# Optimization experiments

Measured on AMD Instinct MI355X. Metric: run time of the kernel, lower is better.

Reference implementation:

```python
import jax, jax.numpy as jnp
import numpy as np

N_NODES = 100000
N_EDGES = 1600000
D = 128


def setup_inputs() -> dict:
    key = jax.random.key(0)
    k1, k2, k3, k4, k5 = jax.random.split(key, 5)
    x = jax.random.normal(k1, (N_NODES, D), dtype=jnp.float32)
    edge_index = jax.random.randint(k2, (2, N_EDGES), 0, N_NODES, dtype=jnp.int32)
    edge_weight = jax.random.uniform(k3, (N_EDGES,), dtype=jnp.float32)
    W_lin = jax.random.normal(k4, (D, D), dtype=jnp.float32) / np.sqrt(D)
    W_gcn = jax.random.normal(k5, (D, D), dtype=jnp.float32) / np.sqrt(D)
    return {"x": x, "edge_index": edge_index, "edge_weight": edge_weight,
            "W_lin": W_lin, "W_gcn": W_gcn}


def reference(x, edge_index, edge_weight, W_lin, W_gcn):
    # hl = Linear(x) (no bias)
    hl = x @ W_lin  # [N, D]

    # GCNConv with add_self_loops=False, normalize=True, no bias:
    row = edge_index[0]  # src
    col = edge_index[1]  # dst
    # symmetric gcn_norm from edge weights (degree scattered onto dst)
    deg = jax.ops.segment_sum(edge_weight, col, num_segments=x.shape[0])  # [N]
    deg_inv_sqrt = jnp.where(deg > 0, jax.lax.rsqrt(deg), 0.0)
    norm = deg_inv_sqrt[row] * edge_weight * deg_inv_sqrt[col]  # [E]

    h = x @ W_gcn  # [N, D] transform before propagate
    msg = h[row] * norm[:, None]  # [E, D] gather + scale
    hr = jax.ops.segment_sum(msg, col, num_segments=x.shape[0])  # scatter-add [N, D]

    return hl + hr
```

## Files before the change

kernel.cpp:

```cpp
#include <hip/hip_runtime.h>

#define NN 100000
#define NE 1600000
#define DD 128
#define NB 1563
#define HIST_BLKS 128
#define PB (HIST_BLKS / 64)
#define CAST_BLKS 752
#define WT2_BLKS  16
#define K1_BLKS (HIST_BLKS + CAST_BLKS + WT2_BLKS)
#define BINCAP 1536

typedef __attribute__((ext_vector_type(8))) short bf16x8;
typedef __attribute__((ext_vector_type(4))) float f32x4;

__device__ inline unsigned short f2bf(float f) {
  union { float f; unsigned u; } v; v.f = f;
  unsigned r = (v.u + 0x7FFF + ((v.u >> 16) & 1)) >> 16;
  return (unsigned short)r;
}

__global__ __launch_bounds__(512) void kb1(const int* __restrict__ col,
    const float* __restrict__ x, const float* __restrict__ Wl, const float* __restrict__ Wg,
    unsigned* __restrict__ hist, unsigned short* __restrict__ xb, unsigned short* __restrict__ WT2) {
  __shared__ unsigned h1[NB];
  int b = blockIdx.x, tid = threadIdx.x;
  if (b < HIST_BLKS) {
    for (int i = tid; i < NB; i += 512) h1[i] = 0;
    __syncthreads();
    for (int e = b * 512 + tid; e < NE; e += HIST_BLKS * 512)
      atomicAdd(&h1[((unsigned)col[e]) >> 6], 1u);
    __syncthreads();
    for (int i = tid; i < NB; i += 512) hist[(size_t)i * HIST_BLKS + b] = h1[i];
  } else if (b < HIST_BLKS + CAST_BLKS) {
    int bb = b - HIST_BLKS;
    const int total8 = NN * DD / 8;
    for (int i = bb * 512 + tid; i < total8; i += CAST_BLKS * 512) {
      float4 a = *(const float4*)&x[i * 8];
      float4 q = *(const float4*)&x[i * 8 + 4];
      unsigned short o[8] = {f2bf(a.x), f2bf(a.y), f2bf(a.z), f2bf(a.w),
                             f2bf(q.x), f2bf(q.y), f2bf(q.z), f2bf(q.w)};
      *(uint4*)&xb[i * 8] = *(uint4*)o;
    }
  } else {
    int bb = b - HIST_BLKS - CAST_BLKS;
    int j = bb * 8 + (tid >> 6);
    int l = tid & 63;
    for (int k = l; k < 256; k += 64) {
      const float* W = (k < DD) ? Wl : Wg;
      WT2[j * 256 + k] = f2bf(W[(k & (DD - 1)) * DD + j]);
    }
  }
}

__global__ __launch_bounds__(256) void kb2a(const unsigned* __restrict__ hist,
    unsigned* __restrict__ binTotal) {
  int w = (blockIdx.x * 256 + threadIdx.x) >> 6, l = threadIdx.x & 63;
  if (w >= NB) return;
  unsigned s = 0;
  for (int k = l; k < HIST_BLKS; k += 64) s += hist[(size_t)w * HIST_BLKS + k];
  #pragma unroll
  for (int off = 32; off >= 1; off >>= 1) s += __shfl_down(s, off, 64);
  if (l == 0) binTotal[w] = s;
}

__global__ __launch_bounds__(512) void kb2b(const unsigned* __restrict__ binTotal,
    unsigned* __restrict__ binBase) {
  __shared__ unsigned ps[512];
  int t = threadIdx.x;
  unsigned v[4], s = 0;
  #pragma unroll
  for (int k = 0; k < 4; k++) { int i = t * 4 + k; v[k] = (i < NB) ? binTotal[i] : 0; s += v[k]; }
  ps[t] = s;
  __syncthreads();
  for (int off = 1; off < 512; off <<= 1) {
    unsigned u = (t >= off) ? ps[t - off] : 0;
    __syncthreads();
    ps[t] += u;
    __syncthreads();
  }
  unsigned run = ps[t] - s;
  #pragma unroll
  for (int k = 0; k < 4; k++) { int i = t * 4 + k; if (i < NB + 1) binBase[i] = run; run += v[k]; }
}

__global__ __launch_bounds__(256) void kb2c(const unsigned* __restrict__ hist,
    const unsigned* __restrict__ binBase, unsigned* __restrict__ off) {
  int w = (blockIdx.x * 256 + threadIdx.x) >> 6, l = threadIdx.x & 63;
  if (w >= NB) return;
  unsigned v[PB], s = 0;
  #pragma unroll
  for (int k = 0; k < PB; k++) { v[k] = hist[(size_t)w * HIST_BLKS + l * PB + k]; s += v[k]; }
  unsigned incl = s;
  #pragma unroll
  for (int o = 1; o < 64; o <<= 1) { unsigned tt = __shfl_up(incl, o, 64); if (l >= o) incl += tt; }
  unsigned run = binBase[w] + incl - s;
  #pragma unroll
  for (int k = 0; k < PB; k++) { off[(size_t)(l * PB + k) * NB + w] = run; run += v[k]; }
}

__global__ __launch_bounds__(512) void kb3(const int* __restrict__ row, const int* __restrict__ col,
    const float* __restrict__ ew, const unsigned* __restrict__ off,
    unsigned long long* __restrict__ entries) {
  __shared__ unsigned cnt[NB];
  int b = blockIdx.x, tid = threadIdx.x;
  for (int i = tid; i < NB; i += 512) cnt[i] = off[(size_t)b * NB + i];
  __syncthreads();
  for (int e = b * 512 + tid; e < NE; e += HIST_BLKS * 512) {
    int c = col[e];
    unsigned pos = atomicAdd(&cnt[((unsigned)c) >> 6], 1u);
    entries[pos] = ((unsigned long long)__float_as_uint(ew[e]) << 32)
                 | ((unsigned)row[e] << 6) | (unsigned)(c & 63);
  }
}

__global__ __launch_bounds__(256) void kb4(const unsigned long long* __restrict__ entries,
    const unsigned* __restrict__ binBase, float* __restrict__ dis) {
  __shared__ unsigned degFx[64];
  int bin = blockIdx.x, tid = threadIdx.x;
  if (tid < 64) degFx[tid] = 0;
  __syncthreads();
  unsigned s0 = binBase[bin], n = binBase[bin + 1] - s0;
  for (unsigned i = tid; i < n; i += 256) {
    unsigned long long e = entries[s0 + i];
    float w = __uint_as_float((unsigned)(e >> 32));
    atomicAdd(&degFx[(unsigned)e & 63], (unsigned)(w * 67108864.0f + 0.5f));
  }
  __syncthreads();
  if (tid < 64) {
    int node = bin * 64 + tid;
    if (node < NN) {
      float d = (float)degFx[tid] * (1.0f / 67108864.0f);
      dis[node] = (d > 0.0f) ? rsqrtf(d) : 0.0f;
    }
  }
}

__global__ __launch_bounds__(512) void kb5(const unsigned long long* __restrict__ entries,
    const unsigned* __restrict__ binBase, const float* __restrict__ dis,
    const unsigned short* __restrict__ xb, unsigned short* __restrict__ yb) {
  __shared__ unsigned long long raw[BINCAP], srt[BINCAP];
  __shared__ unsigned short rnk[BINCAP];
  __shared__ unsigned cnt64[64];
  __shared__ unsigned base64[64];
  int bin = blockIdx.x, tid = threadIdx.x;
  unsigned s0 = binBase[bin];
  int n = (int)(binBase[bin + 1] - s0);
  if (n > BINCAP) n = BINCAP;
  if (tid < 64) cnt64[tid] = 0;
  for (int i = tid; i < n; i += 512) raw[i] = entries[s0 + i];
  __syncthreads();
  for (int i = tid; i < n; i += 512)
    rnk[i] = (unsigned short)atomicAdd(&cnt64[(unsigned)raw[i] & 63], 1u);
  __syncthreads();
  if (tid < 64) {
    unsigned v = cnt64[tid], incl = v;
    #pragma unroll
    for (int o = 1; o < 64; o <<= 1) { unsigned t2 = __shfl_up(incl, o, 64); if (tid >= o) incl += t2; }
    base64[tid] = incl - v;
  }
  __syncthreads();
  for (int i = tid; i < n; i += 512) {
    unsigned long long e = raw[i];
    srt[base64[(unsigned)e & 63] + rnk[i]] = e;
  }
  __syncthreads();
  for (int i = tid; i < n; i += 512) {
    unsigned long long e = srt[i];
    unsigned src = ((unsigned)e) >> 6;
    float wn = __uint_as_float((unsigned)(e >> 32)) * dis[src];
    srt[i] = ((unsigned long long)__float_as_uint(wn) << 32) | (unsigned)(e & 0xFFFFFFFFu);
  }
  __syncthreads();
  int wv = tid >> 6, lane = tid & 63, grp = lane >> 4, l16 = lane & 15;
  for (int dd = 0; dd < 8; ++dd) {
    int d = wv * 8 + dd;
    int c = bin * 64 + d;
    if (c >= NN) break;
    int e0 = base64[d], m = cnt64[d];
    float acc[8] = {};
    for (int i = 0; i < m; i += 16) {
      int j0 = i + grp, j1 = i + 4 + grp, j2 = i + 8 + grp, j3 = i + 12 + grp;
      unsigned sA = 0, sB = 0, sC = 0, sD = 0;
      float wA = 0.f, wB = 0.f, wC = 0.f, wD = 0.f;
      if (j0 < m) { unsigned long long e = srt[e0 + j0]; sA = ((unsigned)e) >> 6; wA = __uint_as_float((unsigned)(e >> 32)); }
      if (j1 < m) { unsigned long long e = srt[e0 + j1]; sB = ((unsigned)e) >> 6; wB = __uint_as_float((unsigned)(e >> 32)); }
      if (j2 < m) { unsigned long long e = srt[e0 + j2]; sC = ((unsigned)e) >> 6; wC = __uint_as_float((unsigned)(e >> 32)); }
      if (j3 < m) { unsigned long long e = srt[e0 + j3]; sD = ((unsigned)e) >> 6; wD = __uint_as_float((unsigned)(e >> 32)); }
      uint4 qA = *(const uint4*)&xb[(size_t)sA * DD + l16 * 8];
      uint4 qB = *(const uint4*)&xb[(size_t)sB * DD + l16 * 8];
      uint4 qC = *(const uint4*)&xb[(size_t)sC * DD + l16 * 8];
      uint4 qD = *(const uint4*)&xb[(size_t)sD * DD + l16 * 8];
      union { uint4 v; unsigned u[4]; } ua, ub, uc, ud;
      ua.v = qA; ub.v = qB; uc.v = qC; ud.v = qD;
      #pragma unroll
      for (int k = 0; k < 4; k++) {
        union { unsigned u; float f; } lo, hi;
        lo.u = ua.u[k] << 16;          hi.u = ua.u[k] & 0xFFFF0000u;
        acc[2 * k] += wA * lo.f;       acc[2 * k + 1] += wA * hi.f;
        lo.u = ub.u[k] << 16;          hi.u = ub.u[k] & 0xFFFF0000u;
        acc[2 * k] += wB * lo.f;       acc[2 * k + 1] += wB * hi.f;
        lo.u = uc.u[k] << 16;          hi.u = uc.u[k] & 0xFFFF0000u;
        acc[2 * k] += wC * lo.f;       acc[2 * k + 1] += wC * hi.f;
        lo.u = ud.u[k] << 16;          hi.u = ud.u[k] & 0xFFFF0000u;
        acc[2 * k] += wD * lo.f;       acc[2 * k + 1] += wD * hi.f;
      }
    }
    #pragma unroll
    for (int k = 0; k < 8; k++) {
      acc[k] += __shfl_xor(acc[k], 16, 64);
      acc[k] += __shfl_xor(acc[k], 32, 64);
    }
    if (grp == 0) {
      float dc = dis[c];
      unsigned short o[8] = {f2bf(acc[0] * dc), f2bf(acc[1] * dc), f2bf(acc[2] * dc),
                             f2bf(acc[3] * dc), f2bf(acc[4] * dc), f2bf(acc[5] * dc),
                             f2bf(acc[6] * dc), f2bf(acc[7] * dc)};
      *(uint4*)&yb[(size_t)c * DD + l16 * 8] = *(uint4*)o;
    }
  }
}

__global__ __launch_bounds__(256) void k_gemm(const unsigned short* __restrict__ xb,
    const unsigned short* __restrict__ yb, const unsigned short* __restrict__ WT2,
    float* __restrict__ out, int N) {
  __shared__ __align__(16) unsigned short Bl[128 * 256];
  __shared__ __align__(16) unsigned short Al[64 * 256];
  int t = threadIdx.x;
  int rowbase = blockIdx.x * 64;

  const uint4* WTv = (const uint4*)WT2;
  #pragma unroll
  for (int i = 0; i < 16; i++) {
    int ci = t + i * 256;
    int j = ci >> 5, c16 = ci & 31;
    uint4 v = WTv[ci];
    int byte = j * 512 + c16 * 16;
    byte ^= (j & 7) << 4;
    *(uint4*)((char*)Bl + byte) = v;
  }
  #pragma unroll
  for (int i = 0; i < 8; i++) {
    int ci = t + i * 256;
    int r = ci >> 5, c16 = ci & 31;
    int gr = rowbase + r;
    uint4 v = make_uint4(0, 0, 0, 0);
    if (gr < N) {
      if (c16 < 16) v = *(const uint4*)&xb[(size_t)gr * DD + c16 * 8];
      else          v = *(const uint4*)&yb[(size_t)gr * DD + (c16 - 16) * 8];
    }
    int byte = r * 512 + c16 * 16;
    byte ^= (r & 7) << 4;
    *(uint4*)((char*)Al + byte) = v;
  }
  __syncthreads();

  int wid = t >> 6, lane = t & 63;
  int wn = wid * 32;
  int l15 = lane & 15, l4 = lane >> 4;
  f32x4 acc[4][2] = {};
  #pragma unroll
  for (int kk = 0; kk < 8; kk++) {
    bf16x8 af[4], bfr[2];
    #pragma unroll
    for (int m = 0; m < 4; m++) {
      int r = m * 16 + l15;
      int byte = r * 512 + kk * 64 + l4 * 16;
      byte ^= (r & 7) << 4;
      af[m] = *(const bf16x8*)((const char*)Al + byte);
    }
    #pragma unroll
    for (int n = 0; n < 2; n++) {
      int r = wn + n * 16 + l15;
      int byte = r * 512 + kk * 64 + l4 * 16;
      byte ^= (r & 7) << 4;
      bfr[n] = *(const bf16x8*)((const char*)Bl + byte);
    }
    #pragma unroll
    for (int m = 0; m < 4; m++)
      #pragma unroll
      for (int n = 0; n < 2; n++)
        acc[m][n] = __builtin_amdgcn_mfma_f32_16x16x32_bf16(af[m], bfr[n], acc[m][n], 0, 0, 0);
  }

  #pragma unroll
  for (int m = 0; m < 4; m++) {
    int gr0 = rowbase + m * 16 + l4 * 4;
    #pragma unroll
    for (int n = 0; n < 2; n++) {
      int gc = wn + n * 16 + l15;
      #pragma unroll
      for (int j = 0; j < 4; j++) {
        int gr = gr0 + j;
        if (gr < N) __builtin_nontemporal_store(acc[m][n][j], &out[(size_t)gr * DD + gc]);
      }
    }
  }
}

extern "C" void kernel_launch(void* const* d_in, const int* in_sizes, int n_in,
                              void* d_out, int out_size, void* d_ws, size_t ws_size,
                              hipStream_t stream) {
  const float* x  = (const float*)d_in[0];
  const int*   ei = (const int*)d_in[1];
  const float* ew = (const float*)d_in[2];
  const float* Wl = (const float*)d_in[3];
  const float* Wg = (const float*)d_in[4];
  float* out = (float*)d_out;
  const int* row = ei;
  const int* col = ei + NE;

  const size_t MB = 1u << 20;
  char* base = (char*)d_ws;
  unsigned* hist     = (unsigned*)(base);
  unsigned* off      = (unsigned*)(base + 2 * MB);
  unsigned* binTotal = (unsigned*)(base + 4 * MB);
  unsigned* binBase  = (unsigned*)(base + 4 * MB + 32768);
  unsigned long long* entries = (unsigned long long*)(base + 5 * MB);
  float* dis = (float*)(base + 18 * MB);
  unsigned short* xb = (unsigned short*)(base + 19 * MB);
  unsigned short* yb = (unsigned short*)(base + 45 * MB);
  unsigned short* WT2 = (unsigned short*)(base + 71 * MB);

  kb1<<<K1_BLKS, 512, 0, stream>>>(col, x, Wl, Wg, hist, xb, WT2);
  kb2a<<<(NB + 3) / 4, 256, 0, stream>>>(hist, binTotal);
  kb2b<<<1, 512, 0, stream>>>(binTotal, binBase);
  kb2c<<<(NB + 3) / 4, 256, 0, stream>>>(hist, binBase, off);
  kb3<<<HIST_BLKS, 512, 0, stream>>>(row, col, ew, off, entries);
  kb4<<<NB, 256, 0, stream>>>(entries, binBase, dis);
  kb5<<<NB, 512, 0, stream>>>(entries, binBase, dis, xb, yb);
  k_gemm<<<(NN + 63) / 64, 256, 0, stream>>>(xb, yb, WT2, out, NN);
}
```

Before: 171.3 us.

## Restructure gather-aggregate kernel: fewer threads, single-pass bin sort, nontemporal stores

The per-bin aggregation kernel moves from 512 to 256 threads and drops the raw staging buffer and rank array. It counts destinations straight from global memory, then scatters entries into sorted shared-memory order with a second atomic counter, folding the source-degree scaling into the same pass. Each wave now handles 16 destinations and issues two row gathers per iteration instead of four, and the entry writes and output writes use nontemporal stores. This cuts shared memory use and one sort pass, so more blocks can be resident, but entries are read from global memory twice and each wave has less memory-level parallelism in flight.

```diff
diff --git a/kernel.cpp b/kernel.cpp
--- a/kernel.cpp
+++ b/kernel.cpp
@@ -13,6 +13,7 @@
 
 typedef __attribute__((ext_vector_type(8))) short bf16x8;
 typedef __attribute__((ext_vector_type(4))) float f32x4;
+typedef __attribute__((ext_vector_type(4))) unsigned u32x4;
 
 __device__ inline unsigned short f2bf(float f) {
   union { float f; unsigned u; } v; v.f = f;
@@ -109,8 +110,9 @@
   for (int e = b * 512 + tid; e < NE; e += HIST_BLKS * 512) {
     int c = col[e];
     unsigned pos = atomicAdd(&cnt[((unsigned)c) >> 6], 1u);
-    entries[pos] = ((unsigned long long)__float_as_uint(ew[e]) << 32)
-                 | ((unsigned)row[e] << 6) | (unsigned)(c & 63);
+    unsigned long long v = ((unsigned long long)__float_as_uint(ew[e]) << 32)
+                         | ((unsigned)row[e] << 6) | (unsigned)(c & 63);
+    __builtin_nontemporal_store(v, &entries[pos]);
   }
 }
 
@@ -136,22 +138,19 @@
   }
 }
 
-__global__ __launch_bounds__(512) void kb5(const unsigned long long* __restrict__ entries,
+__global__ __launch_bounds__(256) void kb5(const unsigned long long* __restrict__ entries,
     const unsigned* __restrict__ binBase, const float* __restrict__ dis,
     const unsigned short* __restrict__ xb, unsigned short* __restrict__ yb) {
-  __shared__ unsigned long long raw[BINCAP], srt[BINCAP];
-  __shared__ unsigned short rnk[BINCAP];
-  __shared__ unsigned cnt64[64];
-  __shared__ unsigned base64[64];
+  __shared__ unsigned long long srt[BINCAP];
+  __shared__ unsigned cnt64[64], base64[64], run64[64];
   int bin = blockIdx.x, tid = threadIdx.x;
   unsigned s0 = binBase[bin];
   int n = (int)(binBase[bin + 1] - s0);
   if (n > BINCAP) n = BINCAP;
-  if (tid < 64) cnt64[tid] = 0;
-  for (int i = tid; i < n; i += 512) raw[i] = entries[s0 + i];
-  __syncthreads();
-  for (int i = tid; i < n; i += 512)
-    rnk[i] = (unsigned short)atomicAdd(&cnt64[(unsigned)raw[i] & 63], 1u);
+  if (tid < 64) { cnt64[tid] = 0; run64[tid] = 0; }
+  __syncthreads();
+  for (int i = tid; i < n; i += 256)
+    atomicAdd(&cnt64[(unsigned)entries[s0 + i] & 63], 1u);
   __syncthreads();
   if (tid < 64) {
     unsigned v = cnt64[tid], incl = v;
@@ -160,50 +159,39 @@
     base64[tid] = incl - v;
   }
   __syncthreads();
-  for (int i = tid; i < n; i += 512) {
-    unsigned long long e = raw[i];
-    srt[base64[(unsigned)e & 63] + rnk[i]] = e;
-  }
-  __syncthreads();
-  for (int i = tid; i < n; i += 512) {
-    unsigned long long e = srt[i];
+  for (int i = tid; i < n; i += 256) {
+    unsigned long long e = __builtin_nontemporal_load(&entries[s0 + i]);
+    unsigned d = (unsigned)e & 63;
+    unsigned pos = base64[d] + atomicAdd(&run64[d], 1u);
     unsigned src = ((unsigned)e) >> 6;
     float wn = __uint_as_float((unsigned)(e >> 32)) * dis[src];
-    srt[i] = ((unsigned long long)__float_as_uint(wn) << 32) | (unsigned)(e & 0xFFFFFFFFu);
+    srt[pos] = ((unsigned long long)__float_as_uint(wn) << 32) | src;
   }
   __syncthreads();
   int wv = tid >> 6, lane = tid & 63, grp = lane >> 4, l16 = lane & 15;
-  for (int dd = 0; dd < 8; ++dd) {
-    int d = wv * 8 + dd;
+  for (int dd = 0; dd < 16; ++dd) {
+    int d = wv * 16 + dd;
     int c = bin * 64 + d;
     if (c >= NN) break;
     int e0 = base64[d], m = cnt64[d];
     float acc[8] = {};
-    for (int i = 0; i < m; i += 16) {
-      int j0 = i + grp, j1 = i + 4 + grp, j2 = i + 8 + grp, j3 = i + 12 + grp;
-      unsigned sA = 0, sB = 0, sC = 0, sD = 0;
-      float wA = 0.f, wB = 0.f, wC = 0.f, wD = 0.f;
-      if (j0 < m) { unsigned long long e = srt[e0 + j0]; sA = ((unsigned)e) >> 6; wA = __uint_as_float((unsigned)(e >> 32)); }
-      if (j1 < m) { unsigned long long e = srt[e0 + j1]; sB = ((unsigned)e) >> 6; wB = __uint_as_float((unsigned)(e >> 32)); }
-      if (j2 < m) { unsigned long long e = srt[e0 + j2]; sC = ((unsigned)e) >> 6; wC = __uint_as_float((unsigned)(e >> 32)); }
-      if (j3 < m) { unsigned long long e = srt[e0 + j3]; sD = ((unsigned)e) >> 6; wD = __uint_as_float((unsigned)(e >> 32)); }
-      uint4 qA = *(const uint4*)&xb[(size_t)sA * DD + l16 * 8];
-      uint4 qB = *(const uint4*)&xb[(size_t)sB * DD + l16 * 8];
-      uint4 qC = *(const uint4*)&xb[(size_t)sC * DD + l16 * 8];
-      uint4 qD = *(const uint4*)&xb[(size_t)sD * DD + l16 * 8];
-      union { uint4 v; unsigned u[4]; } ua, ub, uc, ud;
-      ua.v = qA; ub.v = qB; uc.v = qC; ud.v = qD;
+    for (int i = 0; i < m; i += 8) {
+      int ja = i + grp, jb = i + 4 + grp;
+      unsigned sa = 0, sb = 0;
+      float wa = 0.f, wb = 0.f;
+      if (ja < m) { unsigned long long e = srt[e0 + ja]; sa = (unsigned)e; wa = __uint_as_float((unsigned)(e >> 32)); }
+      if (jb < m) { unsigned long long e = srt[e0 + jb]; sb = (unsigned)e; wb = __uint_as_float((unsigned)(e >> 32)); }
+      uint4 qA = *(const uint4*)&xb[(size_t)sa * DD + l16 * 8];
+      uint4 qB = *(const uint4*)&xb[(size_t)sb * DD + l16 * 8];
+      union { uint4 v; unsigned u[4]; } ua, ub;
+      ua.v = qA; ub.v = qB;
       #pragma unroll
       for (int k = 0; k < 4; k++) {
         union { unsigned u; float f; } lo, hi;
         lo.u = ua.u[k] << 16;          hi.u = ua.u[k] & 0xFFFF0000u;
-        acc[2 * k] += wA * lo.f;       acc[2 * k + 1] += wA * hi.f;
+        acc[2 * k] += wa * lo.f;       acc[2 * k + 1] += wa * hi.f;
         lo.u = ub.u[k] << 16;          hi.u = ub.u[k] & 0xFFFF0000u;
-        acc[2 * k] += wB * lo.f;       acc[2 * k + 1] += wB * hi.f;
-        lo.u = uc.u[k] << 16;          hi.u = uc.u[k] & 0xFFFF0000u;
-        acc[2 * k] += wC * lo.f;       acc[2 * k + 1] += wC * hi.f;
-        lo.u = ud.u[k] << 16;          hi.u = ud.u[k] & 0xFFFF0000u;
-        acc[2 * k] += wD * lo.f;       acc[2 * k + 1] += wD * hi.f;
+        acc[2 * k] += wb * lo.f;       acc[2 * k + 1] += wb * hi.f;
       }
     }
     #pragma unroll
@@ -216,7 +204,12 @@
       unsigned short o[8] = {f2bf(acc[0] * dc), f2bf(acc[1] * dc), f2bf(acc[2] * dc),
                              f2bf(acc[3] * dc), f2bf(acc[4] * dc), f2bf(acc[5] * dc),
                              f2bf(acc[6] * dc), f2bf(acc[7] * dc)};
-      *(uint4*)&yb[(size_t)c * DD + l16 * 8] = *(uint4*)o;
+      u32x4 ov;
+      ov.x = ((unsigned)o[1] << 16) | o[0];
+      ov.y = ((unsigned)o[3] << 16) | o[2];
+      ov.z = ((unsigned)o[5] << 16) | o[4];
+      ov.w = ((unsigned)o[7] << 16) | o[6];
+      __builtin_nontemporal_store(ov, (u32x4*)&yb[(size_t)c * DD + l16 * 8]);
     }
   }
 }
@@ -328,6 +321,6 @@
   kb2c<<<(NB + 3) / 4, 256, 0, stream>>>(hist, binBase, off);
   kb3<<<HIST_BLKS, 512, 0, stream>>>(row, col, ew, off, entries);
   kb4<<<NB, 256, 0, stream>>>(entries, binBase, dis);
-  kb5<<<NB, 512, 0, stream>>>(entries, binBase, dis, xb, yb);
+  kb5<<<NB, 256, 0, stream>>>(entries, binBase, dis, xb, yb);
   k_gemm<<<(NN + 63) / 64, 256, 0, stream>>>(xb, yb, WT2, out, NN);
 }
```

After: 191.0 us. 1.11x slower.
